# Kernel optimization log

Measured on AMD Instinct MI355X. Metric: run time of the kernel, lower is better.

## Reference

```python
import jax, jax.numpy as jnp
import numpy as np

B, T, D = 32, 512, 1024


def setup_inputs() -> dict:
    key = jax.random.key(0)
    ks = jax.random.split(key, 10)
    s = 1.0 / np.sqrt(D)
    return {
        "x": jax.random.normal(ks[0], (B, T, D), jnp.float32),
        "W1": jax.random.normal(ks[1], (D, D), jnp.float32) * s,
        "b1": jax.random.normal(ks[2], (D,), jnp.float32) * s,
        "W2": jax.random.normal(ks[3], (D, D), jnp.float32) * s,
        "b2": jax.random.normal(ks[4], (D,), jnp.float32) * s,
        "W3": jax.random.normal(ks[5], (D, D), jnp.float32) * s,
        "b3": jax.random.normal(ks[6], (D,), jnp.float32) * s,
        "W4": jax.random.normal(ks[7], (D, D), jnp.float32) * s,
        "b4": jax.random.normal(ks[8], (D,), jnp.float32) * s,
        "bias": jax.random.normal(ks[9], (1, D), jnp.float32),
    }


def _lstm(x, W1, b1, W2, b2, W3, b3, W4, b4, bias):
    # Fuse the four D->D gate projections into one [D,4D] matmul per step.
    # nn.Linear computes s @ W^T + b; weights here are stored as [out,in]=[D,D].
    Wcat = jnp.concatenate([W1.T, W2.T, W3.T, W4.T], axis=1)        # [D, 4D]
    bcat = jnp.concatenate([b1, b2, b3, b4]) + jnp.tile(bias[0], 4)  # [4D]

    def step(carry, xt):
        c, h = carry                      # cellState (hiddenUp), hidden (hiddenDown): [B,D]
        s = h + xt                        # sum_ = hiddenDown + xt
        z = s @ Wcat + bcat               # [B,4D]
        zf, zi, zg, zo = jnp.split(z, 4, axis=1)
        f = jax.nn.sigmoid(zf)            # forgetGate
        i = jax.nn.sigmoid(zi) * jnp.tanh(zg)  # inputGate
        c = c * f + i                     # cellUpdate
        h = jax.nn.sigmoid(zo) * jnp.tanh(c)   # outputGate -> hiddenDown
        return (c, h), h

    c0 = jnp.zeros((x.shape[0], x.shape[2]), x.dtype)
    h0 = jnp.zeros_like(c0)
    (cT, hT), ys = jax.lax.scan(step, (c0, h0), jnp.swapaxes(x, 0, 1))
    out = jnp.swapaxes(ys, 0, 1)          # [B,T,D]
    return out, cT[:, None, :], hT[:, None, :]


def reference(x, W1, b1, W2, b2, W3, b3, W4, b4, bias):
    return _lstm(x, W1, b1, W2, b2, W3, b3, W4, b4, bias)
```

## Files before the change

kernel.cpp:

```cpp
#include <hip/hip_runtime.h>
#include <hip/hip_bf16.h>

#define NBLK 64
#define NTHR 256

typedef __attribute__((ext_vector_type(8))) short short8;
typedef __attribute__((ext_vector_type(4))) float f32x4;

constexpr int B = 32, T = 512, D = 1024;
constexpr int JW = D / NBLK;
constexpr int KW = D / 4;
static_assert(JW * NBLK == D, "partition");


__device__ __forceinline__ unsigned short f2bf(float f) {
  unsigned u = __builtin_bit_cast(unsigned, f);
  u += 0x7FFFu + ((u >> 16) & 1u);
  return (unsigned short)(u >> 16);
}

__device__ __forceinline__ float sigm(float v) {
  return 1.0f / (1.0f + __expf(-v));
}

__device__ __forceinline__ float tanh_fast(float v) {
  v = fminf(fmaxf(v, -30.0f), 30.0f);
  float e = __expf(2.0f * v);
  return (e - 1.0f) / (e + 1.0f);
}

__device__ __forceinline__ void st_u32_llc(unsigned* p, unsigned v) {
  asm volatile("global_store_dword %0, %1, off sc0 sc1" :: "v"(p), "v"(v) : "memory");
}

struct u32x4s { unsigned x, y, z, w; };

__global__ void __launch_bounds__(NTHR, 1) lstm_persistent(
    const float* __restrict__ x,
    const float* __restrict__ W1, const float* __restrict__ b1,
    const float* __restrict__ W2, const float* __restrict__ b2,
    const float* __restrict__ W3, const float* __restrict__ b3,
    const float* __restrict__ W4, const float* __restrict__ b4,
    const float* __restrict__ bias,
    float* __restrict__ out,
    unsigned* __restrict__ sq)
{
  __shared__ float zx[2][4][B][72];

  const int blk  = blockIdx.x;
  const int tid  = threadIdx.x;
  const int wv   = tid >> 6;
  const int lane = tid & 63;
  const int j0   = blk * JW;
  const int rot  = blk & 7;

  const int m     = lane & 15;
  const int kg    = (lane >> 4) * 8;
  const int kbase = wv * KW;

  const float* Wg[4] = {W1, W2, W3, W4};
  short8 bfrag[4][8];
#pragma unroll
  for (int g = 0; g < 4; ++g) {
    const float* wrow = Wg[g] + (size_t)(j0 + m) * D + kbase;
#pragma unroll
    for (int kk = 0; kk < 8; ++kk) {
      const int kkr = (kk + rot) & 7;
      float4 fa = *(const float4*)(wrow + kkr * 32 + kg);
      float4 fb = *(const float4*)(wrow + kkr * 32 + kg + 4);
      short8 v;
      v[0] = (short)f2bf(fa.x); v[1] = (short)f2bf(fa.y);
      v[2] = (short)f2bf(fa.z); v[3] = (short)f2bf(fa.w);
      v[4] = (short)f2bf(fb.x); v[5] = (short)f2bf(fb.y);
      v[6] = (short)f2bf(fb.z); v[7] = (short)f2bf(fb.w);
      bfrag[g][kk] = v;
    }
  }

  const int gb   = tid >> 3;
  const int jp   = (tid & 7) * 2;
  const int jcol = j0 + jp;

  const float bsum0 = bias[jcol], bsum1 = bias[jcol + 1];
  const float bf0 = b1[jcol] + bsum0, bf1 = b1[jcol + 1] + bsum1;
  const float bi0 = b2[jcol] + bsum0, bi1 = b2[jcol + 1] + bsum1;
  const float bg0 = b3[jcol] + bsum0, bg1 = b3[jcol + 1] + bsum1;
  const float bo0 = b4[jcol] + bsum0, bo1 = b4[jcol + 1] + bsum1;

  const float* xrow = x + (size_t)gb * T * D + jcol;
  float* outrow     = out + (size_t)gb * T * D + jcol;
  float* cTp        = out + (size_t)B * T * D + (size_t)gb * D + jcol;
  float* hTp        = cTp + (size_t)B * D;

  {
    float2 x0 = *(const float2*)xrow;
    unsigned v = ((unsigned)f2bf(x0.x) | ((unsigned)f2bf(x0.y) << 16)) & ~1u;
    st_u32_llc(sq + blk * 256 + tid, v);
  }

  const int aoff = ((kbase >> 4) + (kg >> 4)) * 512 + m * 16 + (kg & 8);

  float c0 = 0.0f, c1 = 0.0f;

  for (int t = 0; t < T; ++t) {
    const int tn = (t + 1 < T) ? (t + 1) : (T - 1);
    float2 xv;
    asm volatile("global_load_dwordx2 %0, %1, off"
                 : "=v"(xv) : "v"(xrow + (size_t)tn * D));

    const unsigned short* ap =
        (const unsigned short*)sq + (size_t)(t & 3) * 32768 + aoff;
    const unsigned eexp = (unsigned)(t >> 2) & 1u;
    short8 a0[8], a1[8];
    f32x4 acc[2][4];

#pragma unroll
    for (int kk = 0; kk < 8; ++kk) {
      const int kkr = (kk + rot) & 7;
      asm volatile("global_load_dwordx4 %0, %1, off sc0 sc1"
                   : "=v"(a0[kk]) : "v"(ap + kkr * 1024));
      asm volatile("global_load_dwordx4 %0, %1, off sc0 sc1"
                   : "=v"(a1[kk]) : "v"(ap + kkr * 1024 + 256));
    }
#pragma unroll
    for (int mt = 0; mt < 2; ++mt)
#pragma unroll
      for (int g = 0; g < 4; ++g) acc[mt][g] = (f32x4){0.f, 0.f, 0.f, 0.f};

    unsigned orv = 0u, andv = 0xFFFFFFFFu;
#define MFMA_KK(kk, NSTR)                                                     \
    asm volatile("s_waitcnt vmcnt(" NSTR ")" ::: "memory");                   \
    __builtin_amdgcn_sched_barrier(0);                                        \
    _Pragma("unroll")                                                         \
    for (int g = 0; g < 4; ++g) {                                             \
      acc[0][g] = __builtin_amdgcn_mfma_f32_16x16x32_bf16(a0[kk], bfrag[g][kk], acc[0][g], 0, 0, 0); \
      acc[1][g] = __builtin_amdgcn_mfma_f32_16x16x32_bf16(a1[kk], bfrag[g][kk], acc[1][g], 0, 0, 0); \
    }                                                                         \
    {                                                                         \
      u32x4s q0 = __builtin_bit_cast(u32x4s, a0[kk]);                         \
      u32x4s q1 = __builtin_bit_cast(u32x4s, a1[kk]);                         \
      orv  |= q0.x | q0.y | q0.z | q0.w | q1.x | q1.y | q1.z | q1.w;          \
      andv &= q0.x & q0.y & q0.z & q0.w & q1.x & q1.y & q1.z & q1.w;          \
    }
    MFMA_KK(0, "14") MFMA_KK(1, "12") MFMA_KK(2, "10") MFMA_KK(3, "8")
    MFMA_KK(4, "6")  MFMA_KK(5, "4")  MFMA_KK(6, "2")  MFMA_KK(7, "0")
#undef MFMA_KK

    {
      unsigned bad = eexp ? (~andv & 1u) : (orv & 1u);
      if (!__all((int)(bad == 0u))) {
        int guard = 0;
        for (;;) {
#pragma unroll
          for (int kk = 0; kk < 8; ++kk) {
            const int kkr = (kk + rot) & 7;
            asm volatile("global_load_dwordx4 %0, %1, off sc0 sc1"
                         : "=v"(a0[kk]) : "v"(ap + kkr * 1024));
            asm volatile("global_load_dwordx4 %0, %1, off sc0 sc1"
                         : "=v"(a1[kk]) : "v"(ap + kkr * 1024 + 256));
          }
          asm volatile("s_waitcnt vmcnt(0)" ::: "memory");
          __builtin_amdgcn_sched_barrier(0);
          unsigned o2 = 0u, a2 = 0xFFFFFFFFu;
#pragma unroll
          for (int kk = 0; kk < 8; ++kk) {
            u32x4s q0 = __builtin_bit_cast(u32x4s, a0[kk]);
            u32x4s q1 = __builtin_bit_cast(u32x4s, a1[kk]);
            o2 |= q0.x | q0.y | q0.z | q0.w | q1.x | q1.y | q1.z | q1.w;
            a2 &= q0.x & q0.y & q0.z & q0.w & q1.x & q1.y & q1.z & q1.w;
          }
          unsigned b2 = eexp ? (~a2 & 1u) : (o2 & 1u);
          if (__all((int)(b2 == 0u))) break;
          if (++guard > (1 << 12)) break;
        }
#pragma unroll
        for (int mt = 0; mt < 2; ++mt)
#pragma unroll
          for (int g = 0; g < 4; ++g) acc[mt][g] = (f32x4){0.f, 0.f, 0.f, 0.f};
#pragma unroll
        for (int kk = 0; kk < 8; ++kk)
#pragma unroll
          for (int g = 0; g < 4; ++g) {
            acc[0][g] = __builtin_amdgcn_mfma_f32_16x16x32_bf16(a0[kk], bfrag[g][kk], acc[0][g], 0, 0, 0);
            acc[1][g] = __builtin_amdgcn_mfma_f32_16x16x32_bf16(a1[kk], bfrag[g][kk], acc[1][g], 0, 0, 0);
          }
      }
    }

    const int pz = t & 1;
    {
      const int zr = (lane >> 4) * 4;
#pragma unroll
      for (int g = 0; g < 4; ++g)
#pragma unroll
        for (int r = 0; r < 4; ++r) {
          zx[pz][wv][zr + r][g * 16 + m]      = acc[0][g][r];
          zx[pz][wv][zr + r + 16][g * 16 + m] = acc[1][g][r];
        }
    }
    __syncthreads();

    float zf0, zf1, zi0, zi1, zg0, zg1, zo0, zo1;
    {
      float2 f_ = *(const float2*)&zx[pz][0][gb][jp];
      float2 i_ = *(const float2*)&zx[pz][0][gb][16 + jp];
      float2 g_ = *(const float2*)&zx[pz][0][gb][32 + jp];
      float2 o_ = *(const float2*)&zx[pz][0][gb][48 + jp];
      zf0 = f_.x; zf1 = f_.y; zi0 = i_.x; zi1 = i_.y;
      zg0 = g_.x; zg1 = g_.y; zo0 = o_.x; zo1 = o_.y;
#pragma unroll
      for (int w = 1; w < 4; ++w) {
        f_ = *(const float2*)&zx[pz][w][gb][jp];
        i_ = *(const float2*)&zx[pz][w][gb][16 + jp];
        g_ = *(const float2*)&zx[pz][w][gb][32 + jp];
        o_ = *(const float2*)&zx[pz][w][gb][48 + jp];
        zf0 += f_.x; zf1 += f_.y; zi0 += i_.x; zi1 += i_.y;
        zg0 += g_.x; zg1 += g_.y; zo0 += o_.x; zo1 += o_.y;
      }
    }

    float f0 = sigm(zf0 + bf0), f1 = sigm(zf1 + bf1);
    float i0 = sigm(zi0 + bi0) * tanh_fast(zg0 + bg0);
    float i1 = sigm(zi1 + bi1) * tanh_fast(zg1 + bg1);
    c0 = c0 * f0 + i0;
    c1 = c1 * f1 + i1;
    float h0 = sigm(zo0 + bo0) * tanh_fast(c0);
    float h1 = sigm(zo1 + bo1) * tanh_fast(c1);

    if (t + 1 < T) {
      const unsigned epub = (unsigned)((t + 1) >> 2) & 1u;
      unsigned v = (((unsigned)f2bf(h0 + xv.x) |
                     ((unsigned)f2bf(h1 + xv.y) << 16)) & ~1u) | epub;
      st_u32_llc(sq + (size_t)((t + 1) & 3) * 16384 + blk * 256 + tid, v);
      *(float2*)(outrow + (size_t)t * D) = make_float2(h0, h1);
    } else {
      *(float2*)(outrow + (size_t)t * D) = make_float2(h0, h1);
      *(float2*)cTp = make_float2(c0, c1);
      *(float2*)hTp = make_float2(h0, h1);
    }

    asm volatile("" :: "v"(xv));
  }
}

extern "C" void kernel_launch(void* const* d_in, const int* in_sizes, int n_in,
                              void* d_out, int out_size, void* d_ws, size_t ws_size,
                              hipStream_t stream) {
  const float* x    = (const float*)d_in[0];
  const float* W1   = (const float*)d_in[1];
  const float* b1   = (const float*)d_in[2];
  const float* W2   = (const float*)d_in[3];
  const float* b2   = (const float*)d_in[4];
  const float* W3   = (const float*)d_in[5];
  const float* b3   = (const float*)d_in[6];
  const float* W4   = (const float*)d_in[7];
  const float* b4   = (const float*)d_in[8];
  const float* bias = (const float*)d_in[9];

  unsigned* sq = (unsigned*)d_ws;

  hipMemsetAsync(d_ws, 0xFF, 262144, stream);
  hipLaunchKernelGGL(lstm_persistent, dim3(NBLK), dim3(NTHR), 0, stream,
                     x, W1, b1, W2, b2, W3, b3, W4, b4, bias,
                     (float*)d_out, sq);
}
```

Baseline: 1.587 ms.

## Add per-wave step-counter flags for cross-block sync and defer MFMA until data valid

Adds a small array of per-block, per-wave step counters that each block publishes after writing its hidden state. When the epoch-bit check on the loaded hidden state fails, consumers now spin on these counters with double-buffered polls before reloading the data. The hidden-state ring shrinks from four slots to two, and the MFMA accumulation moves after validation, so it runs once per step instead of speculatively and then again on failure. This trades extra flag stores and a second memset for cheaper polling and no wasted MFMA work. Moving MFMA out of the load pipeline may expose load latency on the fast path.

```diff
diff --git a/kernel.cpp b/kernel.cpp
--- a/kernel.cpp
+++ b/kernel.cpp
@@ -43,6 +43,7 @@
     const float* __restrict__ W4, const float* __restrict__ b4,
     const float* __restrict__ bias,
     float* __restrict__ out,
+    unsigned* __restrict__ flags,
     unsigned* __restrict__ sq)
 {
   __shared__ float zx[2][4][B][72];
@@ -96,11 +97,14 @@
     float2 x0 = *(const float2*)xrow;
     unsigned v = ((unsigned)f2bf(x0.x) | ((unsigned)f2bf(x0.y) << 16)) & ~1u;
     st_u32_llc(sq + blk * 256 + tid, v);
+    if (lane < 8) st_u32_llc(flags + lane * 256 + 4 * blk + wv, 1u);
   }
 
   const int aoff = ((kbase >> 4) + (kg >> 4)) * 512 + m * 16 + (kg & 8);
+  const unsigned* pollp = flags + rot * 256 + 64 * wv + lane;
 
   float c0 = 0.0f, c1 = 0.0f;
+  unsigned rA = 0, rB = 0;
 
   for (int t = 0; t < T; ++t) {
     const int tn = (t + 1 < T) ? (t + 1) : (T - 1);
@@ -109,10 +113,9 @@
                  : "=v"(xv) : "v"(xrow + (size_t)tn * D));
 
     const unsigned short* ap =
-        (const unsigned short*)sq + (size_t)(t & 3) * 32768 + aoff;
-    const unsigned eexp = (unsigned)(t >> 2) & 1u;
+        (const unsigned short*)sq + (size_t)(t & 1) * 32768 + aoff;
+    const unsigned eexp = (unsigned)(t >> 1) & 1u;
     short8 a0[8], a1[8];
-    f32x4 acc[2][4];
 
 #pragma unroll
     for (int kk = 0; kk < 8; ++kk) {
@@ -122,34 +125,37 @@
       asm volatile("global_load_dwordx4 %0, %1, off sc0 sc1"
                    : "=v"(a1[kk]) : "v"(ap + kkr * 1024 + 256));
     }
-#pragma unroll
-    for (int mt = 0; mt < 2; ++mt)
-#pragma unroll
-      for (int g = 0; g < 4; ++g) acc[mt][g] = (f32x4){0.f, 0.f, 0.f, 0.f};
-
     unsigned orv = 0u, andv = 0xFFFFFFFFu;
-#define MFMA_KK(kk, NSTR)                                                     \
+#define CHK_KK(kk, NSTR)                                                      \
     asm volatile("s_waitcnt vmcnt(" NSTR ")" ::: "memory");                   \
     __builtin_amdgcn_sched_barrier(0);                                        \
-    _Pragma("unroll")                                                         \
-    for (int g = 0; g < 4; ++g) {                                             \
-      acc[0][g] = __builtin_amdgcn_mfma_f32_16x16x32_bf16(a0[kk], bfrag[g][kk], acc[0][g], 0, 0, 0); \
-      acc[1][g] = __builtin_amdgcn_mfma_f32_16x16x32_bf16(a1[kk], bfrag[g][kk], acc[1][g], 0, 0, 0); \
-    }                                                                         \
     {                                                                         \
       u32x4s q0 = __builtin_bit_cast(u32x4s, a0[kk]);                         \
       u32x4s q1 = __builtin_bit_cast(u32x4s, a1[kk]);                         \
       orv  |= q0.x | q0.y | q0.z | q0.w | q1.x | q1.y | q1.z | q1.w;          \
       andv &= q0.x & q0.y & q0.z & q0.w & q1.x & q1.y & q1.z & q1.w;          \
     }
-    MFMA_KK(0, "14") MFMA_KK(1, "12") MFMA_KK(2, "10") MFMA_KK(3, "8")
-    MFMA_KK(4, "6")  MFMA_KK(5, "4")  MFMA_KK(6, "2")  MFMA_KK(7, "0")
-#undef MFMA_KK
-
+    CHK_KK(0, "14") CHK_KK(1, "12") CHK_KK(2, "10") CHK_KK(3, "8")
+    CHK_KK(4, "6")  CHK_KK(5, "4")  CHK_KK(6, "2")  CHK_KK(7, "0")
+#undef CHK_KK
     {
       unsigned bad = eexp ? (~andv & 1u) : (orv & 1u);
       if (!__all((int)(bad == 0u))) {
+        const unsigned tgt = (unsigned)(t + 1);
         int guard = 0;
+        asm volatile("global_load_dword %0, %1, off sc0 sc1" : "=v"(rA) : "v"(pollp));
+        for (;;) {
+          asm volatile("global_load_dword %0, %1, off sc0 sc1" : "=v"(rB) : "v"(pollp));
+          asm volatile("s_waitcnt vmcnt(1)" ::: "memory");
+          __builtin_amdgcn_sched_barrier(0);
+          if (__all((int)(rA >= tgt))) break;
+          asm volatile("global_load_dword %0, %1, off sc0 sc1" : "=v"(rA) : "v"(pollp));
+          asm volatile("s_waitcnt vmcnt(1)" ::: "memory");
+          __builtin_amdgcn_sched_barrier(0);
+          if (__all((int)(rB >= tgt))) break;
+          if (++guard > (1 << 21)) break;
+        }
+        int g2 = 0;
         for (;;) {
 #pragma unroll
           for (int kk = 0; kk < 8; ++kk) {
@@ -171,21 +177,24 @@
           }
           unsigned b2 = eexp ? (~a2 & 1u) : (o2 & 1u);
           if (__all((int)(b2 == 0u))) break;
-          if (++guard > (1 << 12)) break;
+          if (++g2 > (1 << 12)) break;
         }
-#pragma unroll
-        for (int mt = 0; mt < 2; ++mt)
-#pragma unroll
-          for (int g = 0; g < 4; ++g) acc[mt][g] = (f32x4){0.f, 0.f, 0.f, 0.f};
-#pragma unroll
-        for (int kk = 0; kk < 8; ++kk)
-#pragma unroll
-          for (int g = 0; g < 4; ++g) {
-            acc[0][g] = __builtin_amdgcn_mfma_f32_16x16x32_bf16(a0[kk], bfrag[g][kk], acc[0][g], 0, 0, 0);
-            acc[1][g] = __builtin_amdgcn_mfma_f32_16x16x32_bf16(a1[kk], bfrag[g][kk], acc[1][g], 0, 0, 0);
-          }
       }
     }
+    __builtin_amdgcn_sched_barrier(0);
+
+    f32x4 acc[2][4];
+#pragma unroll
+    for (int mt = 0; mt < 2; ++mt)
+#pragma unroll
+      for (int g = 0; g < 4; ++g) acc[mt][g] = (f32x4){0.f, 0.f, 0.f, 0.f};
+#pragma unroll
+    for (int kk = 0; kk < 8; ++kk)
+#pragma unroll
+      for (int g = 0; g < 4; ++g) {
+        acc[0][g] = __builtin_amdgcn_mfma_f32_16x16x32_bf16(a0[kk], bfrag[g][kk], acc[0][g], 0, 0, 0);
+        acc[1][g] = __builtin_amdgcn_mfma_f32_16x16x32_bf16(a1[kk], bfrag[g][kk], acc[1][g], 0, 0, 0);
+      }
 
     const int pz = t & 1;
     {
@@ -228,10 +237,11 @@
     float h1 = sigm(zo1 + bo1) * tanh_fast(c1);
 
     if (t + 1 < T) {
-      const unsigned epub = (unsigned)((t + 1) >> 2) & 1u;
+      const unsigned epub = (unsigned)((t + 1) >> 1) & 1u;
       unsigned v = (((unsigned)f2bf(h0 + xv.x) |
                      ((unsigned)f2bf(h1 + xv.y) << 16)) & ~1u) | epub;
-      st_u32_llc(sq + (size_t)((t + 1) & 3) * 16384 + blk * 256 + tid, v);
+      st_u32_llc(sq + (size_t)((t + 1) & 1) * 16384 + blk * 256 + tid, v);
+      if (lane < 8) st_u32_llc(flags + lane * 256 + 4 * blk + wv, (unsigned)(t + 2));
       *(float2*)(outrow + (size_t)t * D) = make_float2(h0, h1);
     } else {
       *(float2*)(outrow + (size_t)t * D) = make_float2(h0, h1);
@@ -239,7 +249,7 @@
       *(float2*)hTp = make_float2(h0, h1);
     }
 
-    asm volatile("" :: "v"(xv));
+    asm volatile("" :: "v"(rA), "v"(rB), "v"(xv));
   }
 }
 
@@ -257,10 +267,12 @@
   const float* b4   = (const float*)d_in[8];
   const float* bias = (const float*)d_in[9];
 
-  unsigned* sq = (unsigned*)d_ws;
-
-  hipMemsetAsync(d_ws, 0xFF, 262144, stream);
+  unsigned* flags = (unsigned*)d_ws;
+  unsigned* sq    = (unsigned*)((char*)d_ws + 8192);
+
+  hipMemsetAsync(d_ws, 0, 8192, stream);
+  hipMemsetAsync((char*)d_ws + 8192, 0xFF, 131072, stream);
   hipLaunchKernelGGL(lstm_persistent, dim3(NBLK), dim3(NTHR), 0, stream,
                      x, W1, b1, W2, b2, W3, b3, W4, b4, bias,
-                     (float*)d_out, sq);
-}
+                     (float*)d_out, flags, sq);
+}
```

New measurement: 1.704 ms. 7.3% more time.

## Shrink the handoff ring to two slots and retry only stale K-chunks

Applied to the files above, without the earlier changes.

Each block's published hidden state now goes into a 2-slot ring instead of 4 slots. The parity bit embedded in the data flips every 2 steps so stale and fresh values stay distinguishable, and the workspace memset is halved. The spin-wait is restructured so each K-chunk is checked separately. Chunks that are ready run their MFMAs right away, and only the stale chunks are reloaded and retried. Before, all 16 loads were reloaded and the whole MFMA sum was recomputed. This is meant to cut retry latency and memory traffic on the critical per-step path, at the cost of more branching and tighter ring reuse.

```diff
diff --git a/kernel.cpp b/kernel.cpp
--- a/kernel.cpp
+++ b/kernel.cpp
@@ -101,6 +101,7 @@
   const int aoff = ((kbase >> 4) + (kg >> 4)) * 512 + m * 16 + (kg & 8);
 
   float c0 = 0.0f, c1 = 0.0f;
+  short8 a0[8], a1[8];
 
   for (int t = 0; t < T; ++t) {
     const int tn = (t + 1 < T) ? (t + 1) : (T - 1);
@@ -109,10 +110,8 @@
                  : "=v"(xv) : "v"(xrow + (size_t)tn * D));
 
     const unsigned short* ap =
-        (const unsigned short*)sq + (size_t)(t & 3) * 32768 + aoff;
-    const unsigned eexp = (unsigned)(t >> 2) & 1u;
-    short8 a0[8], a1[8];
-    f32x4 acc[2][4];
+        (const unsigned short*)sq + (size_t)(t & 1) * 32768 + aoff;
+    const unsigned eexp = (unsigned)(t >> 1) & 1u;
 
 #pragma unroll
     for (int kk = 0; kk < 8; ++kk) {
@@ -122,70 +121,69 @@
       asm volatile("global_load_dwordx4 %0, %1, off sc0 sc1"
                    : "=v"(a1[kk]) : "v"(ap + kkr * 1024 + 256));
     }
+
+    f32x4 acc[2][4];
 #pragma unroll
     for (int mt = 0; mt < 2; ++mt)
 #pragma unroll
       for (int g = 0; g < 4; ++g) acc[mt][g] = (f32x4){0.f, 0.f, 0.f, 0.f};
 
-    unsigned orv = 0u, andv = 0xFFFFFFFFu;
-#define MFMA_KK(kk, NSTR)                                                     \
-    asm volatile("s_waitcnt vmcnt(" NSTR ")" ::: "memory");                   \
-    __builtin_amdgcn_sched_barrier(0);                                        \
+    unsigned pend = 0u;
+
+#define PAIR_OK(kk, OKVAR)                                                    \
+    {                                                                         \
+      u32x4s q0 = __builtin_bit_cast(u32x4s, a0[kk]);                         \
+      u32x4s q1 = __builtin_bit_cast(u32x4s, a1[kk]);                         \
+      unsigned orv  = q0.x | q0.y | q0.z | q0.w | q1.x | q1.y | q1.z | q1.w;  \
+      unsigned andv = q0.x & q0.y & q0.z & q0.w & q1.x & q1.y & q1.z & q1.w;  \
+      unsigned bad = eexp ? (~andv & 1u) : (orv & 1u);                        \
+      OKVAR = __all((int)(bad == 0u));                                        \
+    }
+#define MFMA_PAIR(kk)                                                         \
     _Pragma("unroll")                                                         \
     for (int g = 0; g < 4; ++g) {                                             \
       acc[0][g] = __builtin_amdgcn_mfma_f32_16x16x32_bf16(a0[kk], bfrag[g][kk], acc[0][g], 0, 0, 0); \
       acc[1][g] = __builtin_amdgcn_mfma_f32_16x16x32_bf16(a1[kk], bfrag[g][kk], acc[1][g], 0, 0, 0); \
-    }                                                                         \
+    }
+#define STEP_KK(kk, NSTR)                                                     \
+    asm volatile("s_waitcnt vmcnt(" NSTR ")" ::: "memory");                   \
+    __builtin_amdgcn_sched_barrier(0);                                        \
     {                                                                         \
-      u32x4s q0 = __builtin_bit_cast(u32x4s, a0[kk]);                         \
-      u32x4s q1 = __builtin_bit_cast(u32x4s, a1[kk]);                         \
-      orv  |= q0.x | q0.y | q0.z | q0.w | q1.x | q1.y | q1.z | q1.w;          \
-      andv &= q0.x & q0.y & q0.z & q0.w & q1.x & q1.y & q1.z & q1.w;          \
-    }
-    MFMA_KK(0, "14") MFMA_KK(1, "12") MFMA_KK(2, "10") MFMA_KK(3, "8")
-    MFMA_KK(4, "6")  MFMA_KK(5, "4")  MFMA_KK(6, "2")  MFMA_KK(7, "0")
-#undef MFMA_KK
+      int ok_;                                                                \
+      PAIR_OK(kk, ok_)                                                        \
+      if (ok_) { MFMA_PAIR(kk) } else { pend |= (1u << kk); }                 \
+    }
+    STEP_KK(0, "14") STEP_KK(1, "12") STEP_KK(2, "10") STEP_KK(3, "8")
+    STEP_KK(4, "6")  STEP_KK(5, "4")  STEP_KK(6, "2")  STEP_KK(7, "0")
+#undef STEP_KK
 
     {
-      unsigned bad = eexp ? (~andv & 1u) : (orv & 1u);
-      if (!__all((int)(bad == 0u))) {
-        int guard = 0;
-        for (;;) {
-#pragma unroll
-          for (int kk = 0; kk < 8; ++kk) {
+      int guard = 0;
+      while (pend) {
+#pragma unroll
+        for (int kk = 0; kk < 8; ++kk)
+          if (pend & (1u << kk)) {
             const int kkr = (kk + rot) & 7;
             asm volatile("global_load_dwordx4 %0, %1, off sc0 sc1"
                          : "=v"(a0[kk]) : "v"(ap + kkr * 1024));
             asm volatile("global_load_dwordx4 %0, %1, off sc0 sc1"
                          : "=v"(a1[kk]) : "v"(ap + kkr * 1024 + 256));
           }
-          asm volatile("s_waitcnt vmcnt(0)" ::: "memory");
-          __builtin_amdgcn_sched_barrier(0);
-          unsigned o2 = 0u, a2 = 0xFFFFFFFFu;
-#pragma unroll
-          for (int kk = 0; kk < 8; ++kk) {
-            u32x4s q0 = __builtin_bit_cast(u32x4s, a0[kk]);
-            u32x4s q1 = __builtin_bit_cast(u32x4s, a1[kk]);
-            o2 |= q0.x | q0.y | q0.z | q0.w | q1.x | q1.y | q1.z | q1.w;
-            a2 &= q0.x & q0.y & q0.z & q0.w & q1.x & q1.y & q1.z & q1.w;
+        asm volatile("s_waitcnt vmcnt(0)" ::: "memory");
+        __builtin_amdgcn_sched_barrier(0);
+#pragma unroll
+        for (int kk = 0; kk < 8; ++kk)
+          if (pend & (1u << kk)) {
+            int ok_;
+            PAIR_OK(kk, ok_)
+            if (ok_) { MFMA_PAIR(kk) pend &= ~(1u << kk); }
           }
-          unsigned b2 = eexp ? (~a2 & 1u) : (o2 & 1u);
-          if (__all((int)(b2 == 0u))) break;
-          if (++guard > (1 << 12)) break;
-        }
-#pragma unroll
-        for (int mt = 0; mt < 2; ++mt)
-#pragma unroll
-          for (int g = 0; g < 4; ++g) acc[mt][g] = (f32x4){0.f, 0.f, 0.f, 0.f};
-#pragma unroll
-        for (int kk = 0; kk < 8; ++kk)
-#pragma unroll
-          for (int g = 0; g < 4; ++g) {
-            acc[0][g] = __builtin_amdgcn_mfma_f32_16x16x32_bf16(a0[kk], bfrag[g][kk], acc[0][g], 0, 0, 0);
-            acc[1][g] = __builtin_amdgcn_mfma_f32_16x16x32_bf16(a1[kk], bfrag[g][kk], acc[1][g], 0, 0, 0);
-          }
+        if (++guard > (1 << 16)) break;
       }
     }
+#undef PAIR_OK
+#undef MFMA_PAIR
+    __builtin_amdgcn_sched_barrier(0);
 
     const int pz = t & 1;
     {
@@ -228,10 +226,10 @@
     float h1 = sigm(zo1 + bo1) * tanh_fast(c1);
 
     if (t + 1 < T) {
-      const unsigned epub = (unsigned)((t + 1) >> 2) & 1u;
+      const unsigned epub = (unsigned)((t + 1) >> 1) & 1u;
       unsigned v = (((unsigned)f2bf(h0 + xv.x) |
                      ((unsigned)f2bf(h1 + xv.y) << 16)) & ~1u) | epub;
-      st_u32_llc(sq + (size_t)((t + 1) & 3) * 16384 + blk * 256 + tid, v);
+      st_u32_llc(sq + (size_t)((t + 1) & 1) * 16384 + blk * 256 + tid, v);
       *(float2*)(outrow + (size_t)t * D) = make_float2(h0, h1);
     } else {
       *(float2*)(outrow + (size_t)t * D) = make_float2(h0, h1);
@@ -259,7 +257,7 @@
 
   unsigned* sq = (unsigned*)d_ws;
 
-  hipMemsetAsync(d_ws, 0xFF, 262144, stream);
+  hipMemsetAsync(d_ws, 0xFF, 131072, stream);
   hipLaunchKernelGGL(lstm_persistent, dim3(NBLK), dim3(NTHR), 0, stream,
                      x, W1, b1, W2, b2, W3, b3, W4, b4, bias,
                      (float*)d_out, sq);
```

After: 1.543 ms (median of 3 runs). -2.8%, faster.
